# Kernel tuning notes

Hardware: AMD Instinct MI355X
Metric: run time of the kernel (lower is better)

The kernel has to match this reference:

```python
import jax, jax.numpy as jnp
import numpy as np

N_VERTS = 2562


def _uniform(key, shape, bound):
    return jax.random.uniform(key, shape, jnp.float32, -bound, bound)


def vert_align(feat, pos):
    # feat: [B,C,H,W]; pos: [B,N,3], xy in [-1,1] -> bilinear sample -> [B,N,C]
    B, C, H, W = feat.shape
    ft = jnp.transpose(feat, (0, 2, 3, 1))  # [B,H,W,C]
    x = (jnp.clip(pos[..., 0], -1.0, 1.0) + 1.0) * 0.5 * (W - 1)
    y = (jnp.clip(pos[..., 1], -1.0, 1.0) + 1.0) * 0.5 * (H - 1)
    x0 = jnp.floor(x)
    y0 = jnp.floor(y)
    x0i = x0.astype(jnp.int32)
    y0i = y0.astype(jnp.int32)
    x1i = jnp.minimum(x0i + 1, W - 1)
    y1i = jnp.minimum(y0i + 1, H - 1)
    wx = (x - x0)[..., None]
    wy = (y - y0)[..., None]
    b = jnp.arange(B)[:, None]
    f00 = ft[b, y0i, x0i]
    f01 = ft[b, y0i, x1i]
    f10 = ft[b, y1i, x0i]
    f11 = ft[b, y1i, x1i]
    return (f00 * (1 - wx) * (1 - wy) + f01 * wx * (1 - wy)
            + f10 * (1 - wx) * wy + f11 * wx * wy)


def graph_conv(x, adj, w0, w1):
    # relu(x @ w0 + adj @ (x @ w1))
    return jax.nn.relu(x @ w0 + jnp.einsum('bij,bjc->bic', adj, x @ w1))


def setup_inputs() -> dict:
    key = jax.random.key(0)
    ks = jax.random.split(key, 20)
    B, N = 8, N_VERTS
    inp = {
        'conv2_3': jax.random.normal(ks[0], (B, 256, 56, 56), jnp.float32),
        'conv3_4': jax.random.normal(ks[1], (B, 512, 28, 28), jnp.float32),
        'conv4_6': jax.random.normal(ks[2], (B, 1024, 14, 14), jnp.float32),
        'conv5_3': jax.random.normal(ks[3], (B, 2048, 7, 7), jnp.float32),
        # scaled so row sums are O(1), like a normalized dense adjacency
        'vertex_adjacency': jax.random.uniform(ks[4], (B, N, N), jnp.float32) * (2.0 / N),
        'vertex_positions': jax.random.uniform(ks[5], (B, N, 3), jnp.float32) * 2.0 - 1.0,
        'vertex_features': jax.random.normal(ks[6], (B, N, 128), jnp.float32),
    }
    # learned parameters (torch default / GraphConv uniform init)
    inp['w_lin0'] = _uniform(ks[7], (3840, 128), 1.0 / np.sqrt(3840))
    inp['b_lin0'] = _uniform(ks[8], (128,), 1.0 / np.sqrt(3840))
    inp['gc0_w0'] = _uniform(ks[9], (259, 131), 1.0 / np.sqrt(259))
    inp['gc0_w1'] = _uniform(ks[10], (259, 131), 1.0 / np.sqrt(259))
    inp['gc1_w0'] = _uniform(ks[11], (131, 128), 1.0 / np.sqrt(131))
    inp['gc1_w1'] = _uniform(ks[12], (131, 128), 1.0 / np.sqrt(131))
    inp['gc2_w0'] = _uniform(ks[13], (131, 128), 1.0 / np.sqrt(131))
    inp['gc2_w1'] = _uniform(ks[14], (131, 128), 1.0 / np.sqrt(131))
    inp['w_lin1'] = _uniform(ks[15], (128, 3), 1.0 / np.sqrt(128))
    inp['b_lin1'] = _uniform(ks[16], (3,), 1.0 / np.sqrt(128))
    return inp


def reference(conv2_3, conv3_4, conv4_6, conv5_3, vertex_adjacency,
              vertex_positions, vertex_features,
              w_lin0, b_lin0, gc0_w0, gc0_w1, gc1_w0, gc1_w1,
              gc2_w0, gc2_w1, w_lin1, b_lin1):
    verts = jnp.concatenate(
        [vert_align(f, vertex_positions)
         for f in (conv2_3, conv3_4, conv4_6, conv5_3)], axis=2)  # [B,N,3840]
    projected = verts @ w_lin0 + b_lin0                             # [B,N,128]
    vf = jnp.concatenate([vertex_features, vertex_positions, projected], axis=2)  # 259
    h = graph_conv(vf, vertex_adjacency, gc0_w0, gc0_w1)            # [B,N,131]
    h = jnp.concatenate([vertex_positions, h], axis=2)              # 134? no: 3+131=134 -- see note
    h = graph_conv(h[:, :, :131] if h.shape[2] != 131 else h, vertex_adjacency, gc1_w0, gc1_w1)
    h = jnp.concatenate([vertex_positions, h], axis=2)              # 131
    new_features = graph_conv(h, vertex_adjacency, gc2_w0, gc2_w1)  # [B,N,128]
    new_positions = vertex_positions + jnp.tanh(new_features @ w_lin1 + b_lin1)
    return new_positions, new_features
```

## Files before the change

kernel.cpp:

```cpp
#include <hip/hip_runtime.h>
#include <hip/hip_bf16.h>

typedef __attribute__((ext_vector_type(8))) short bf16x8;
typedef __attribute__((ext_vector_type(4))) float f32x4;
typedef long long i64;

static __device__ __forceinline__ float bflo(unsigned v){ return __uint_as_float(v << 16); }
static __device__ __forceinline__ float bfhi(unsigned v){ return __uint_as_float(v & 0xffff0000u); }
static __device__ __forceinline__ unsigned short f2bf(float f){
  unsigned u = __float_as_uint(f);
  u += 0x7FFFu + ((u >> 16) & 1u);
  return (unsigned short)(u >> 16);
}
static __device__ __forceinline__ unsigned f2e4m3(float x){
  unsigned b = __float_as_uint(x);
  unsigned s = (b >> 31) << 7;
  b &= 0x7fffffffu;
  if (b >= 0x43e80000u) return s | 0x7eu;
  if (b < 0x3c800000u)
    return s | (unsigned)rintf(__uint_as_float(b) * 512.f);
  unsigned b2 = b + 0x7ffffu + ((b >> 20) & 1u);
  return s | (((b2 >> 23) - 120u) << 3) | ((b2 >> 20) & 7u);
}
static __device__ __forceinline__ unsigned pk4_e4m3(float a, float b, float c, float d){
#if __has_builtin(__builtin_amdgcn_cvt_pk_fp8_f32)
  unsigned r = 0;
  r = (unsigned)__builtin_amdgcn_cvt_pk_fp8_f32(a, b, (int)r, false);
  r = (unsigned)__builtin_amdgcn_cvt_pk_fp8_f32(c, d, (int)r, true);
  return r;
#else
  return f2e4m3(a) | (f2e4m3(b) << 8) | (f2e4m3(c) << 16) | (f2e4m3(d) << 24);
#endif
}
static __device__ __forceinline__ void gload_lds16(const void* g, void* l){
  __builtin_amdgcn_global_load_lds((const __attribute__((address_space(1))) unsigned int*)g,
                                   (__attribute__((address_space(3))) unsigned int*)l, 16, 0, 0);
}

#define MFMA16(acc, a, b) (acc) = __builtin_amdgcn_mfma_f32_16x16x32_bf16((a),(b),(acc),0,0,0)
#define MFMA8(acc, a, b)  (acc) = __builtin_amdgcn_mfma_f32_16x16x32_fp8_fp8((a),(b),(acc),0,0,0)

#define NB    8
#define NVRT  2562
#define MP    2624
#define NRB2  82
#define NRB16 164
#define NKT8  21
#define KOCT  336
#define YO    ((size_t)KOCT*128*8)

#define G_B0 0ul
#define G_B1 3211264ul
#define G_B2 4014080ul
#define G_B3 4214784ul
#define G_TOT 4264960ul

struct PWArgs {
  const float* src[7];
  unsigned short* dst[7];
  int ksrc[7], nsrc[7];
};
__global__ void k_packw_all(PWArgs a)
{
  const int cb[8] = {0,491520,528384,565248,585728,606208,626688,647168};
  int g = blockIdx.x * 256 + threadIdx.x;
#pragma unroll
  for (int s = 0; s < 7; s++){
    if (g >= cb[s] && g < cb[s+1]){
      int li = g - cb[s];
      int k = li >> 7, c = li & 127;
      int ks = a.ksrc[s], ns = a.nsrc[s];
      float v = (k < ks) ? a.src[s][(size_t)k * ns + c] : 0.f;
      a.dst[s][((size_t)(k >> 3) * 128 + c) * 8 + (k & 7)] = f2bf(v);
    }
  }
}

__global__ __launch_bounds__(256) void k_gproj2(
    const float* __restrict__ c0m, const float* __restrict__ c1m,
    const float* __restrict__ c2m, const float* __restrict__ c3m,
    const unsigned short* __restrict__ wp,
    unsigned short* __restrict__ G)
{
  __shared__ f32x4 red[3][1024];
  int bx = blockIdx.x;
  int m, b, tile;
  if (bx < 784)      { m = 0; b = bx / 98;  tile = bx - b*98; }
  else if (bx < 984) { int l = bx-784;  m = 1; b = l / 25; tile = l - b*25; }
  else if (bx < 1040){ int l = bx-984;  m = 2; b = l / 7;  tile = l - b*7; }
  else               { int l = bx-1040; m = 3; b = l >> 1; tile = l & 1; }
  int C  = 256 << m;
  int HW = (m==0)?3136:(m==1)?784:(m==2)?196:49;
  const float* src = ((m==0)?c0m:(m==1)?c1m:(m==2)?c2m:c3m) + (size_t)b * C * HW;
  size_t gb = ((m==0)?G_B0:(m==1)?G_B1:(m==2)?G_B2:G_B3) + (size_t)b * HW * 128;
  int ko8 = (m==0)?0:(m==1)?32:(m==2)?96:224;

  int t = threadIdx.x, w = t >> 6, lane = t & 63;
  int l15 = lane & 15, l4 = lane >> 4;
  int hw0 = tile * 32;
  int ar0 = min(hw0 + l15, HW - 1);
  int ar1 = min(hw0 + 16 + l15, HW - 1);

  f32x4 acc[2][8];
#pragma unroll
  for (int i = 0; i < 2; i++)
#pragma unroll
    for (int j = 0; j < 8; j++) acc[i][j] = (f32x4){0,0,0,0};

  int kq = C >> 2;
  int kbeg = w * kq, klim = kbeg + kq;
  for (int kb = kbeg; kb < klim; kb += 32){
    bf16x8 a0, a1;
#pragma unroll
    for (int j = 0; j < 8; j++){
      int cc = kb + l4*8 + j;
      a0[j] = (short)f2bf(src[(size_t)cc * HW + ar0]);
      a1[j] = (short)f2bf(src[(size_t)cc * HW + ar1]);
    }
    size_t bo = ((size_t)(ko8 + (kb>>3) + l4) * 128 + l15) * 8;
#pragma unroll
    for (int cf = 0; cf < 8; cf++){
      bf16x8 bb = *(const bf16x8*)(wp + bo + cf*128);
      MFMA16(acc[0][cf], a0, bb);
      MFMA16(acc[1][cf], a1, bb);
    }
  }

  if (w){
#pragma unroll
    for (int rf = 0; rf < 2; rf++)
#pragma unroll
      for (int cf = 0; cf < 8; cf++)
        red[w-1][(rf*8+cf)*64 + lane] = acc[rf][cf];
  }
  __syncthreads();
  if (!w){
#pragma unroll
    for (int rf = 0; rf < 2; rf++)
#pragma unroll
      for (int cf = 0; cf < 8; cf++){
        int i = (rf*8+cf)*64 + lane;
        f32x4 s = acc[rf][cf] + red[0][i] + red[1][i] + red[2][i];
        int col = cf*16 + l15;
#pragma unroll
        for (int r = 0; r < 4; r++){
          int hw = hw0 + rf*16 + l4*4 + r;
          if (hw < HW) G[gb + (size_t)hw*128 + col] = f2bf(s[r]);
        }
      }
  }
}

__global__ void k_prep2(const float* __restrict__ vfeat, const float* __restrict__ pos,
                        const unsigned short* __restrict__ G,
                        const float* __restrict__ bias,
                        unsigned short* __restrict__ vf,
                        unsigned short* __restrict__ x1,
                        unsigned short* __restrict__ x2,
                        unsigned char* __restrict__ y1A,
                        unsigned char* __restrict__ y1B)
{
  int b = blockIdx.y;
  if (blockIdx.x == 0){
    unsigned long long* za = (unsigned long long*)(y1A + (size_t)b*YO + (size_t)328*128*8);
    unsigned long long* zb = (unsigned long long*)(y1B + (size_t)b*YO + (size_t)328*128*8);
    int i = threadIdx.x;
#pragma unroll
    for (int j = 0; j < 4; j++){ za[i*4+j] = 0; zb[i*4+j] = 0; }
  }
  int row = blockIdx.x * 4 + (threadIdx.x >> 6);
  int lane = threadIdx.x & 63;
  size_t vfo = ((size_t)b * MP + row) * 288;
  size_t xo  = ((size_t)b * MP + row) * 160;
  if (row < NVRT){
    size_t src = (size_t)b * NVRT + row;
    float px = fminf(fmaxf(pos[src*3 + 0], -1.f), 1.f);
    float py = fminf(fmaxf(pos[src*3 + 1], -1.f), 1.f);
    int c0 = lane * 2;
    float s0 = bias[c0], s1 = bias[c0 + 1];
#pragma unroll
    for (int m = 0; m < 4; m++){
      int W = 56 >> m;
      int HW = W * W;
      size_t gb = (m==0)?G_B0:(m==1)?G_B1:(m==2)?G_B2:G_B3;
      float gx = (px + 1.f) * 0.5f * (float)(W - 1);
      float gy = (py + 1.f) * 0.5f * (float)(W - 1);
      int x0 = (int)floorf(gx), y0 = (int)floorf(gy);
      float wx = gx - (float)x0, wy = gy - (float)y0;
      int x1i = min(x0 + 1, W - 1), y1i = min(y0 + 1, W - 1);
      const unsigned short* g = G + gb + (size_t)b * HW * 128;
      unsigned v00 = *(const unsigned*)(g + ((size_t)(y0 *W + x0 ))*128 + c0);
      unsigned v01 = *(const unsigned*)(g + ((size_t)(y0 *W + x1i))*128 + c0);
      unsigned v10 = *(const unsigned*)(g + ((size_t)(y1i*W + x0 ))*128 + c0);
      unsigned v11 = *(const unsigned*)(g + ((size_t)(y1i*W + x1i))*128 + c0);
      float w00 = (1.f-wx)*(1.f-wy), w01 = wx*(1.f-wy);
      float w10 = (1.f-wx)*wy,       w11 = wx*wy;
      s0 += w00*bflo(v00) + w01*bflo(v01) + w10*bflo(v10) + w11*bflo(v11);
      s1 += w00*bfhi(v00) + w01*bfhi(v01) + w10*bfhi(v10) + w11*bfhi(v11);
    }
    vf[vfo + 131 + c0]     = f2bf(s0);
    vf[vfo + 131 + c0 + 1] = f2bf(s1);
    float2 fv = *(const float2*)(vfeat + src*128 + c0);
    vf[vfo + c0]     = f2bf(fv.x);
    vf[vfo + c0 + 1] = f2bf(fv.y);
    if (lane < 3){
      unsigned short v = f2bf(pos[src*3 + lane]);
      vf[vfo + 128 + lane] = v;
      x1[xo + lane] = v;
      x2[xo + lane] = v;
    }
    if (lane >= 32 && lane < 61) vf[vfo + 259 + (lane - 32)] = 0;
    if (lane < 29){ x1[xo + 131 + lane] = 0; x2[xo + 131 + lane] = 0; }
  } else {
    for (int c = lane; c < 288; c += 64) vf[vfo + c] = 0;
    for (int c = lane; c < 160; c += 64){ x1[xo + c] = 0; x2[xo + c] = 0; }
  }
}

__global__ __launch_bounds__(256) void k_adjpack8(const float* __restrict__ adj,
                                                  unsigned char* __restrict__ adjP)
{
  int bid = blockIdx.x;
  int b = bid & 7, rb = bid >> 3;
  int t = threadIdx.x;
  int r = t >> 4, kseg = t & 15;
  int grow = rb*16 + r;
  bool rv = grow < NVRT;
  const float* arow = adj + ((size_t)b*NVRT + (rv ? grow : 0))*NVRT;
  unsigned char* tb = adjP + (((size_t)b*NRB16 + rb)*NKT8) * 2048;
  int tslot = 128*r + 8*(kseg ^ r);

#pragma unroll 3
  for (int kt = 0; kt < NKT8; ++kt){
    int gk = kt*128 + kseg*8;
    float v[8];
    if (rv && gk + 8 <= NVRT){
      float4 f0 = *(const float4*)(arow + gk);
      float4 f1 = *(const float4*)(arow + gk + 4);
      v[0]=f0.x; v[1]=f0.y; v[2]=f0.z; v[3]=f0.w;
      v[4]=f1.x; v[5]=f1.y; v[6]=f1.z; v[7]=f1.w;
    } else if (rv){
#pragma unroll
      for (int e = 0; e < 8; e++){ int k = gk + e; v[e] = (k < NVRT) ? arow[k] : 0.f; }
    } else {
#pragma unroll
      for (int e = 0; e < 8; e++) v[e] = 0.f;
    }
    unsigned lo = pk4_e4m3(v[0]*1024.f, v[1]*1024.f, v[2]*1024.f, v[3]*1024.f);
    unsigned hi = pk4_e4m3(v[4]*1024.f, v[5]*1024.f, v[6]*1024.f, v[7]*1024.f);
    unsigned long long q = (unsigned long long)lo | ((unsigned long long)hi << 32);
    *(unsigned long long*)(tb + (size_t)kt*2048 + tslot) = q;
  }
}

template<int KX>
__global__ __launch_bounds__(256) void k_y1(
    const unsigned short* __restrict__ x,
    const unsigned short* __restrict__ wp1,
    unsigned char* __restrict__ y1p8)
{
  int bid = blockIdx.x;
  int b = bid & 7, rb = (bid >> 3) * 32;
  int t = threadIdx.x, wave = t >> 6, lane = t & 63;
  int rf = wave & 1, ch = wave >> 1;
  int l15 = lane & 15, l4 = lane >> 4;
  f32x4 a1[4];
#pragma unroll
  for (int c = 0; c < 4; c++) a1[c] = (f32x4){0,0,0,0};
  int row = rb + rf*16 + l15;
  const unsigned short* xp = x + ((size_t)b * MP + row) * KX + l4 * 8;
#pragma unroll
  for (int kb = 0; kb < KX; kb += 32){
    bf16x8 a = *(const bf16x8*)(xp + kb);
    size_t bo = ((size_t)((kb>>3) + l4) * 128 + ch*64 + l15) * 8;
#pragma unroll
    for (int c = 0; c < 4; c++){
      bf16x8 b1 = *(const bf16x8*)(wp1 + bo + c*128);
      MFMA16(a1[c], a, b1);
    }
  }
  unsigned char* yb = y1p8 + (size_t)b * YO;
#pragma unroll
  for (int c = 0; c < 4; c++){
    int col = ch*64 + c*16 + l15;
    int orow0 = rb + rf*16 + l4*4;
    unsigned q = pk4_e4m3(a1[c][0], a1[c][1], a1[c][2], a1[c][3]);
    *(unsigned*)(yb + ((size_t)(orow0 >> 3) * 128 + col) * 8 + (orow0 & 7)) = q;
  }
}

template<int EPI, int KX>
__global__ __launch_bounds__(256) void k_adj8(
    const unsigned char* __restrict__ adjP,
    const unsigned char* __restrict__ y1in,
    const unsigned short* __restrict__ x,
    const unsigned short* __restrict__ wp0,
    const unsigned short* __restrict__ wp1n,
    unsigned char* __restrict__ y1out,
    const float* __restrict__ posg,
    unsigned short* __restrict__ xnext,
    float* __restrict__ outf,
    const float* __restrict__ wl1, const float* __restrict__ bl1,
    float* __restrict__ opos)
{
  __shared__ __align__(16) unsigned char abuf[2][2048];
  __shared__ unsigned short xbuf[EPI == 0 ? 16 : 1][168];
  __shared__ float hbuf[EPI == 1 ? 16 : 1][128];
  int bid = blockIdx.x;
  int b = bid & 7, rb = bid >> 3;
  int t = threadIdx.x, w = t >> 6, lane = t & 63;
  int l15 = lane & 15, l4 = lane >> 4;
  const unsigned char* tb = adjP + (((size_t)b*NRB16 + rb)*NKT8) * 2048;
  const unsigned char* yb = y1in + (size_t)b * YO;

  f32x4 acc[2], accW[2];
  acc[0] = (f32x4){0,0,0,0};  acc[1] = (f32x4){0,0,0,0};
  accW[0] = (f32x4){0,0,0,0}; accW[1] = (f32x4){0,0,0,0};

  auto stage = [&](int kt, int bufi){
    if (w < 2)
      gload_lds16(tb + (size_t)kt*2048 + w*1024 + lane*16, &abuf[bufi][w*1024]);
  };

  stage(0, 0);

  if (EPI == 0){
    if (t < 48){
      int r16 = t / 3, c = t - r16*3;
      int grow = rb*16 + r16;
      xbuf[r16][c] = (grow < NVRT) ? f2bf(posg[((size_t)b*NVRT + grow)*3 + c]) : 0;
    }
    {
      int r16 = t >> 4, c0 = 131 + (t & 15);
      xbuf[r16][c0] = 0;
      if (c0 + 16 < 168) xbuf[r16][c0 + 16] = 0;
      if (c0 + 32 < 168) xbuf[r16][c0 + 32] = 0;
    }
  }

  const unsigned short* xr = x + ((size_t)b*MP + rb*16 + l15)*KX + l4*8;
#pragma unroll
  for (int kb = 0; kb < KX; kb += 32){
    bf16x8 ax = *(const bf16x8*)(xr + kb);
    size_t bo = ((size_t)((kb>>3) + l4)*128 + w*32 + l15)*8;
    MFMA16(accW[0], ax, *(const bf16x8*)(wp0 + bo));
    MFMA16(accW[1], ax, *(const bf16x8*)(wp0 + bo + 128));
  }

  __syncthreads();

  for (int kt = 0; kt < NKT8; ++kt){
    int cur = kt & 1;
    if (kt < NKT8-1) stage(kt+1, cur ^ 1);
    const unsigned char* ab = &abuf[cur][0];
#pragma unroll
    for (int sel = 0; sel < 2; sel++){
#pragma unroll
      for (int ks = 0; ks < 2; ks++){
        int koct = sel*8 + ks*4 + l4;
        i64 a = *(const i64*)(ab + 128*l15 + 8*(koct ^ l15));
        const unsigned char* bp = yb + ((size_t)(kt*16 + koct)*128 + w*32 + l15)*8;
        i64 b0 = *(const i64*)(bp);
        i64 b1 = *(const i64*)(bp + 128);
        MFMA8(acc[0], a, b0);
        MFMA8(acc[1], a, b1);
      }
    }
    __syncthreads();
  }

#pragma unroll
  for (int cf = 0; cf < 2; cf++){
    int col = w*32 + cf*16 + l15;
#pragma unroll
    for (int r = 0; r < 4; r++){
      int row16 = l4*4 + r;
      int row = rb*16 + row16;
      float v = fmaxf(accW[cf][r] + acc[cf][r] * 0.0009765625f, 0.f);
      if (EPI == 0){
        unsigned short hb = f2bf(v);
        if (row < NVRT) xnext[((size_t)b*MP + row)*160 + 3 + col] = hb;
        xbuf[row16][3 + col] = hb;
      } else {
        if (row < NVRT) outf[((size_t)b*NVRT + row)*128 + col] = v;
        hbuf[row16][col] = v;
      }
    }
  }
  __syncthreads();

  if (EPI == 0){
    f32x4 accY[2];
    accY[0] = (f32x4){0,0,0,0}; accY[1] = (f32x4){0,0,0,0};
#pragma unroll
    for (int ks = 0; ks < 5; ks++){
      bf16x8 a = *(const bf16x8*)(&xbuf[l15][ks*32 + l4*8]);
      size_t bo = ((size_t)(ks*4 + l4)*128 + w*32 + l15)*8;
      MFMA16(accY[0], a, *(const bf16x8*)(wp1n + bo));
      MFMA16(accY[1], a, *(const bf16x8*)(wp1n + bo + 128));
    }
    unsigned char* yo = y1out + (size_t)b * YO;
#pragma unroll
    for (int cf = 0; cf < 2; cf++){
      int col = w*32 + cf*16 + l15;
      int orow0 = rb*16 + l4*4;
      unsigned q = pk4_e4m3(accY[cf][0], accY[cf][1], accY[cf][2], accY[cf][3]);
      *(unsigned*)(yo + ((size_t)(orow0 >> 3) * 128 + col) * 8 + (orow0 & 7)) = q;
    }
  } else {
#pragma unroll
    for (int rr = 0; rr < 4; rr++){
      int row16 = w*4 + rr;
      int grow = rb*16 + row16;
      if (grow < NVRT){
        int c0 = lane * 2;
        float v0 = hbuf[row16][c0], v1 = hbuf[row16][c0+1];
        float p[3];
#pragma unroll
        for (int j = 0; j < 3; j++){
          p[j] = v0 * wl1[c0*3 + j] + v1 * wl1[c0*3 + 3 + j];
#pragma unroll
          for (int off = 1; off < 64; off <<= 1)
            p[j] += __shfl_xor(p[j], off);
        }
        if (lane == 0){
          size_t po = ((size_t)b * NVRT + grow) * 3;
#pragma unroll
          for (int j = 0; j < 3; j++)
            opos[po + j] = posg[po + j] + tanhf(p[j] + bl1[j]);
        }
      }
    }
  }
}

extern "C" void kernel_launch(void* const* d_in, const int* in_sizes, int n_in,
                              void* d_out, int out_size, void* d_ws, size_t ws_size,
                              hipStream_t stream)
{
  const float* conv[4] = {(const float*)d_in[0], (const float*)d_in[1],
                          (const float*)d_in[2], (const float*)d_in[3]};
  const float* adj   = (const float*)d_in[4];
  const float* pos   = (const float*)d_in[5];
  const float* vfeat = (const float*)d_in[6];
  const float* wlin0 = (const float*)d_in[7];
  const float* blin0 = (const float*)d_in[8];
  const float* gw[6] = {(const float*)d_in[9],  (const float*)d_in[10],
                        (const float*)d_in[11], (const float*)d_in[12],
                        (const float*)d_in[13], (const float*)d_in[14]};
  const float* wlin1 = (const float*)d_in[15];
  const float* blin1 = (const float*)d_in[16];

  char* ws = (char*)d_ws;
  size_t off = 0;
  auto take = [&](size_t bytes)->char* {
    char* p = ws + off;
    off += (bytes + 255) & ~(size_t)255;
    return p;
  };
  unsigned short* G    = (unsigned short*)take(G_TOT * 2);
  unsigned char*  adjP = (unsigned char*)take((size_t)NB*NRB16*NKT8*2048);
  unsigned short* wl0p = (unsigned short*)take((size_t)3840*128*2);
  unsigned short* w0p0 = (unsigned short*)take((size_t)288*128*2);
  unsigned short* w1p0 = (unsigned short*)take((size_t)288*128*2);
  unsigned short* w0p1 = (unsigned short*)take((size_t)160*128*2);
  unsigned short* w1p1 = (unsigned short*)take((size_t)160*128*2);
  unsigned short* w0p2 = (unsigned short*)take((size_t)160*128*2);
  unsigned short* w1p2 = (unsigned short*)take((size_t)160*128*2);
  unsigned short* vf   = (unsigned short*)take((size_t)NB*MP*288*2);
  unsigned short* x1   = (unsigned short*)take((size_t)NB*MP*160*2);
  unsigned short* x2   = (unsigned short*)take((size_t)NB*MP*160*2);
  unsigned char*  y1A  = (unsigned char*)take((size_t)NB*YO);
  unsigned char*  y1B  = (unsigned char*)take((size_t)NB*YO);

  float* out_pos  = (float*)d_out;
  float* out_feat = out_pos + (size_t)NB*NVRT*3;

  PWArgs pw;
  pw.src[0]=wlin0; pw.dst[0]=wl0p; pw.ksrc[0]=3840; pw.nsrc[0]=128;
  pw.src[1]=gw[0]; pw.dst[1]=w0p0; pw.ksrc[1]=259;  pw.nsrc[1]=131;
  pw.src[2]=gw[1]; pw.dst[2]=w1p0; pw.ksrc[2]=259;  pw.nsrc[2]=131;
  pw.src[3]=gw[2]; pw.dst[3]=w0p1; pw.ksrc[3]=131;  pw.nsrc[3]=128;
  pw.src[4]=gw[3]; pw.dst[4]=w1p1; pw.ksrc[4]=131;  pw.nsrc[4]=128;
  pw.src[5]=gw[4]; pw.dst[5]=w0p2; pw.ksrc[5]=131;  pw.nsrc[5]=128;
  pw.src[6]=gw[5]; pw.dst[6]=w1p2; pw.ksrc[6]=131;  pw.nsrc[6]=128;
  k_packw_all<<<2528, 256, 0, stream>>>(pw);
  k_gproj2<<<1056, 256, 0, stream>>>(conv[0], conv[1], conv[2], conv[3], wl0p, G);
  k_prep2<<<dim3(MP/4, NB), 256, 0, stream>>>(vfeat, pos, G, blin0, vf, x1, x2, y1A, y1B);
  k_y1<288><<<NRB2*NB, 256, 0, stream>>>(vf, w1p0, y1A);
  k_adjpack8<<<NRB16*NB, 256, 0, stream>>>(adj, adjP);
  k_adj8<0,288><<<NRB16*NB, 256, 0, stream>>>(adjP, y1A, vf, w0p0, w1p1, y1B, pos,
                                              x1, nullptr, nullptr, nullptr, nullptr);
  k_adj8<0,160><<<NRB16*NB, 256, 0, stream>>>(adjP, y1B, x1, w0p1, w1p2, y1A, pos,
                                              x2, nullptr, nullptr, nullptr, nullptr);
  k_adj8<1,160><<<NRB16*NB, 256, 0, stream>>>(adjP, y1A, x2, w0p2, nullptr, nullptr, pos,
                                              nullptr, out_feat, wlin1, blin1, out_pos);
  (void)in_sizes; (void)n_in; (void)out_size; (void)ws_size;
}
```

Before: 263.1 us.

## Split adjacency fp8 packing across gproj, prep and y1 launches

```diff
diff --git a/kernel.cpp b/kernel.cpp
--- a/kernel.cpp
+++ b/kernel.cpp
@@ -49,11 +49,49 @@
 #define KOCT  336
 #define YO    ((size_t)KOCT*128*8)
 
+#define AP_G 512
+#define AP_P 512
+#define AP_Y 288
+
 #define G_B0 0ul
 #define G_B1 3211264ul
 #define G_B2 4014080ul
 #define G_B3 4214784ul
 #define G_TOT 4264960ul
+
+static __device__ __forceinline__ void adjpack_slab(int slab, const float* __restrict__ adj,
+                                                    unsigned char* __restrict__ adjP, int t)
+{
+  int b = slab & 7, rb = slab >> 3;
+  int r = t >> 4, kseg = t & 15;
+  int grow = rb*16 + r;
+  bool rv = grow < NVRT;
+  const float* arow = adj + ((size_t)b*NVRT + (rv ? grow : 0))*NVRT;
+  unsigned char* tb = adjP + (((size_t)b*NRB16 + rb)*NKT8) * 2048;
+  int tslot = 128*r + 8*(kseg ^ r);
+
+#pragma unroll 3
+  for (int kt = 0; kt < NKT8; ++kt){
+    int gk = kt*128 + kseg*8;
+    float v[8];
+    if (rv && gk + 8 <= NVRT){
+      float4 f0 = *(const float4*)(arow + gk);
+      float4 f1 = *(const float4*)(arow + gk + 4);
+      v[0]=f0.x; v[1]=f0.y; v[2]=f0.z; v[3]=f0.w;
+      v[4]=f1.x; v[5]=f1.y; v[6]=f1.z; v[7]=f1.w;
+    } else if (rv){
+#pragma unroll
+      for (int e = 0; e < 8; e++){ int k = gk + e; v[e] = (k < NVRT) ? arow[k] : 0.f; }
+    } else {
+#pragma unroll
+      for (int e = 0; e < 8; e++) v[e] = 0.f;
+    }
+    unsigned lo = pk4_e4m3(v[0]*1024.f, v[1]*1024.f, v[2]*1024.f, v[3]*1024.f);
+    unsigned hi = pk4_e4m3(v[4]*1024.f, v[5]*1024.f, v[6]*1024.f, v[7]*1024.f);
+    unsigned long long q = (unsigned long long)lo | ((unsigned long long)hi << 32);
+    *(unsigned long long*)(tb + (size_t)kt*2048 + tslot) = q;
+  }
+}
 
 struct PWArgs {
   const float* src[7];
@@ -76,14 +114,17 @@
   }
 }
 
-__global__ __launch_bounds__(256) void k_gproj2(
+__global__ __launch_bounds__(256) void k_par_gproj(
+    const float* __restrict__ adjSrc, unsigned char* __restrict__ adjP,
     const float* __restrict__ c0m, const float* __restrict__ c1m,
     const float* __restrict__ c2m, const float* __restrict__ c3m,
     const unsigned short* __restrict__ wp,
     unsigned short* __restrict__ G)
 {
   __shared__ f32x4 red[3][1024];
-  int bx = blockIdx.x;
+  int bid = blockIdx.x;
+  if (bid < AP_G){ adjpack_slab(bid, adjSrc, adjP, threadIdx.x); return; }
+  int bx = bid - AP_G;
   int m, b, tile;
   if (bx < 784)      { m = 0; b = bx / 98;  tile = bx - b*98; }
   else if (bx < 984) { int l = bx-784;  m = 1; b = l / 25; tile = l - b*25; }
@@ -151,24 +192,29 @@
   }
 }
 
-__global__ void k_prep2(const float* __restrict__ vfeat, const float* __restrict__ pos,
-                        const unsigned short* __restrict__ G,
-                        const float* __restrict__ bias,
-                        unsigned short* __restrict__ vf,
-                        unsigned short* __restrict__ x1,
-                        unsigned short* __restrict__ x2,
-                        unsigned char* __restrict__ y1A,
-                        unsigned char* __restrict__ y1B)
-{
-  int b = blockIdx.y;
-  if (blockIdx.x == 0){
+__global__ __launch_bounds__(256) void k_par_prep(
+    const float* __restrict__ adjSrc, unsigned char* __restrict__ adjP,
+    const float* __restrict__ vfeat, const float* __restrict__ pos,
+    const unsigned short* __restrict__ G,
+    const float* __restrict__ bias,
+    unsigned short* __restrict__ vf,
+    unsigned short* __restrict__ x1,
+    unsigned short* __restrict__ x2,
+    unsigned char* __restrict__ y1A,
+    unsigned char* __restrict__ y1B)
+{
+  int bid = blockIdx.x;
+  if (bid < AP_P){ adjpack_slab(AP_G + bid, adjSrc, adjP, threadIdx.x); return; }
+  int idx = bid - AP_P;
+  int b = idx & 7, rblk = idx >> 3;
+  if (rblk == 0){
     unsigned long long* za = (unsigned long long*)(y1A + (size_t)b*YO + (size_t)328*128*8);
     unsigned long long* zb = (unsigned long long*)(y1B + (size_t)b*YO + (size_t)328*128*8);
     int i = threadIdx.x;
 #pragma unroll
     for (int j = 0; j < 4; j++){ za[i*4+j] = 0; zb[i*4+j] = 0; }
   }
-  int row = blockIdx.x * 4 + (threadIdx.x >> 6);
+  int row = rblk * 4 + (threadIdx.x >> 6);
   int lane = threadIdx.x & 63;
   size_t vfo = ((size_t)b * MP + row) * 288;
   size_t xo  = ((size_t)b * MP + row) * 160;
@@ -217,50 +263,16 @@
   }
 }
 
-__global__ __launch_bounds__(256) void k_adjpack8(const float* __restrict__ adj,
-                                                  unsigned char* __restrict__ adjP)
-{
-  int bid = blockIdx.x;
-  int b = bid & 7, rb = bid >> 3;
-  int t = threadIdx.x;
-  int r = t >> 4, kseg = t & 15;
-  int grow = rb*16 + r;
-  bool rv = grow < NVRT;
-  const float* arow = adj + ((size_t)b*NVRT + (rv ? grow : 0))*NVRT;
-  unsigned char* tb = adjP + (((size_t)b*NRB16 + rb)*NKT8) * 2048;
-  int tslot = 128*r + 8*(kseg ^ r);
-
-#pragma unroll 3
-  for (int kt = 0; kt < NKT8; ++kt){
-    int gk = kt*128 + kseg*8;
-    float v[8];
-    if (rv && gk + 8 <= NVRT){
-      float4 f0 = *(const float4*)(arow + gk);
-      float4 f1 = *(const float4*)(arow + gk + 4);
-      v[0]=f0.x; v[1]=f0.y; v[2]=f0.z; v[3]=f0.w;
-      v[4]=f1.x; v[5]=f1.y; v[6]=f1.z; v[7]=f1.w;
-    } else if (rv){
-#pragma unroll
-      for (int e = 0; e < 8; e++){ int k = gk + e; v[e] = (k < NVRT) ? arow[k] : 0.f; }
-    } else {
-#pragma unroll
-      for (int e = 0; e < 8; e++) v[e] = 0.f;
-    }
-    unsigned lo = pk4_e4m3(v[0]*1024.f, v[1]*1024.f, v[2]*1024.f, v[3]*1024.f);
-    unsigned hi = pk4_e4m3(v[4]*1024.f, v[5]*1024.f, v[6]*1024.f, v[7]*1024.f);
-    unsigned long long q = (unsigned long long)lo | ((unsigned long long)hi << 32);
-    *(unsigned long long*)(tb + (size_t)kt*2048 + tslot) = q;
-  }
-}
-
-template<int KX>
-__global__ __launch_bounds__(256) void k_y1(
+__global__ __launch_bounds__(256) void k_par_y1(
+    const float* __restrict__ adjSrc, unsigned char* __restrict__ adjP,
     const unsigned short* __restrict__ x,
     const unsigned short* __restrict__ wp1,
     unsigned char* __restrict__ y1p8)
 {
   int bid = blockIdx.x;
-  int b = bid & 7, rb = (bid >> 3) * 32;
+  if (bid < AP_Y){ adjpack_slab(AP_G + AP_P + bid, adjSrc, adjP, threadIdx.x); return; }
+  int yid = bid - AP_Y;
+  int b = yid & 7, rb = (yid >> 3) * 32;
   int t = threadIdx.x, wave = t >> 6, lane = t & 63;
   int rf = wave & 1, ch = wave >> 1;
   int l15 = lane & 15, l4 = lane >> 4;
@@ -268,9 +280,9 @@
 #pragma unroll
   for (int c = 0; c < 4; c++) a1[c] = (f32x4){0,0,0,0};
   int row = rb + rf*16 + l15;
-  const unsigned short* xp = x + ((size_t)b * MP + row) * KX + l4 * 8;
-#pragma unroll
-  for (int kb = 0; kb < KX; kb += 32){
+  const unsigned short* xp = x + ((size_t)b * MP + row) * 288 + l4 * 8;
+#pragma unroll
+  for (int kb = 0; kb < 288; kb += 32){
     bf16x8 a = *(const bf16x8*)(xp + kb);
     size_t bo = ((size_t)((kb>>3) + l4) * 128 + ch*64 + l15) * 8;
 #pragma unroll
@@ -485,10 +497,11 @@
   pw.src[5]=gw[4]; pw.dst[5]=w0p2; pw.ksrc[5]=131;  pw.nsrc[5]=128;
   pw.src[6]=gw[5]; pw.dst[6]=w1p2; pw.ksrc[6]=131;  pw.nsrc[6]=128;
   k_packw_all<<<2528, 256, 0, stream>>>(pw);
-  k_gproj2<<<1056, 256, 0, stream>>>(conv[0], conv[1], conv[2], conv[3], wl0p, G);
-  k_prep2<<<dim3(MP/4, NB), 256, 0, stream>>>(vfeat, pos, G, blin0, vf, x1, x2, y1A, y1B);
-  k_y1<288><<<NRB2*NB, 256, 0, stream>>>(vf, w1p0, y1A);
-  k_adjpack8<<<NRB16*NB, 256, 0, stream>>>(adj, adjP);
+  k_par_gproj<<<AP_G + 1056, 256, 0, stream>>>(adj, adjP,
+                                               conv[0], conv[1], conv[2], conv[3], wl0p, G);
+  k_par_prep<<<AP_P + 656*NB, 256, 0, stream>>>(adj, adjP,
+                                                vfeat, pos, G, blin0, vf, x1, x2, y1A, y1B);
+  k_par_y1<<<AP_Y + NRB2*NB, 256, 0, stream>>>(adj, adjP, vf, w1p0, y1A);
   k_adj8<0,288><<<NRB16*NB, 256, 0, stream>>>(adjP, y1A, vf, w0p0, w1p1, y1B, pos,
                                               x1, nullptr, nullptr, nullptr, nullptr);
   k_adj8<0,160><<<NRB16*NB, 256, 0, stream>>>(adjP, y1B, x1, w0p1, w1p2, y1A, pos,
```

Measured after the change: 259.7 us. No clear change (-1.3%).

## Fuse y1, adjacency packing and three graph-conv stages into one persistent kernel

Applied to the files above, without the earlier changes.

```diff
diff --git a/kernel.cpp b/kernel.cpp
--- a/kernel.cpp
+++ b/kernel.cpp
@@ -48,12 +48,281 @@
 #define NKT8  21
 #define KOCT  336
 #define YO    ((size_t)KOCT*128*8)
+#define MEGA_GRID 656
 
 #define G_B0 0ul
 #define G_B1 3211264ul
 #define G_B2 4014080ul
 #define G_B3 4214784ul
 #define G_TOT 4264960ul
+
+static __device__ __forceinline__ void gsync(unsigned* ctr){
+  __syncthreads();
+  if (threadIdx.x == 0){
+    __threadfence();
+    atomicAdd(ctr, 1u);
+    while (__hip_atomic_load(ctr, __ATOMIC_ACQUIRE, __HIP_MEMORY_SCOPE_AGENT) < (unsigned)gridDim.x)
+      __builtin_amdgcn_s_sleep(2);
+  }
+  __syncthreads();
+}
+
+static __device__ __forceinline__ void adjpack_slab(int slab, const float* __restrict__ adj,
+                                                    unsigned char* __restrict__ adjP, int t)
+{
+  int b = slab & 7, rb = slab >> 3;
+  int r = t >> 4, kseg = t & 15;
+  int grow = rb*16 + r;
+  bool rv = grow < NVRT;
+  const float* arow = adj + ((size_t)b*NVRT + (rv ? grow : 0))*NVRT;
+  unsigned char* tb = adjP + (((size_t)b*NRB16 + rb)*NKT8) * 2048;
+  int tslot = 128*r + 8*(kseg ^ r);
+
+#pragma unroll 3
+  for (int kt = 0; kt < NKT8; ++kt){
+    int gk = kt*128 + kseg*8;
+    float v[8];
+    if (rv && gk + 8 <= NVRT){
+      float4 f0 = *(const float4*)(arow + gk);
+      float4 f1 = *(const float4*)(arow + gk + 4);
+      v[0]=f0.x; v[1]=f0.y; v[2]=f0.z; v[3]=f0.w;
+      v[4]=f1.x; v[5]=f1.y; v[6]=f1.z; v[7]=f1.w;
+    } else if (rv){
+#pragma unroll
+      for (int e = 0; e < 8; e++){ int k = gk + e; v[e] = (k < NVRT) ? arow[k] : 0.f; }
+    } else {
+#pragma unroll
+      for (int e = 0; e < 8; e++) v[e] = 0.f;
+    }
+    unsigned lo = pk4_e4m3(v[0]*1024.f, v[1]*1024.f, v[2]*1024.f, v[3]*1024.f);
+    unsigned hi = pk4_e4m3(v[4]*1024.f, v[5]*1024.f, v[6]*1024.f, v[7]*1024.f);
+    unsigned long long q = (unsigned long long)lo | ((unsigned long long)hi << 32);
+    *(unsigned long long*)(tb + (size_t)kt*2048 + tslot) = q;
+  }
+}
+
+static __device__ __forceinline__ void y1_body(int yid,
+    const unsigned short* __restrict__ x,
+    const unsigned short* __restrict__ wp1,
+    unsigned char* __restrict__ y1p8)
+{
+  int b = yid & 7, rb = (yid >> 3) * 32;
+  int t = threadIdx.x, wave = t >> 6, lane = t & 63;
+  int rf = wave & 1, ch = wave >> 1;
+  int l15 = lane & 15, l4 = lane >> 4;
+  f32x4 a1[4];
+#pragma unroll
+  for (int c = 0; c < 4; c++) a1[c] = (f32x4){0,0,0,0};
+  int row = rb + rf*16 + l15;
+  const unsigned short* xp = x + ((size_t)b * MP + row) * 288 + l4 * 8;
+#pragma unroll
+  for (int kb = 0; kb < 288; kb += 32){
+    bf16x8 a = *(const bf16x8*)(xp + kb);
+    size_t bo = ((size_t)((kb>>3) + l4) * 128 + ch*64 + l15) * 8;
+#pragma unroll
+    for (int c = 0; c < 4; c++){
+      bf16x8 b1 = *(const bf16x8*)(wp1 + bo + c*128);
+      MFMA16(a1[c], a, b1);
+    }
+  }
+  unsigned char* yb = y1p8 + (size_t)b * YO;
+#pragma unroll
+  for (int c = 0; c < 4; c++){
+    int col = ch*64 + c*16 + l15;
+    int orow0 = rb + rf*16 + l4*4;
+    unsigned q = pk4_e4m3(a1[c][0], a1[c][1], a1[c][2], a1[c][3]);
+    *(unsigned*)(yb + ((size_t)(orow0 >> 3) * 128 + col) * 8 + (orow0 & 7)) = q;
+  }
+}
+
+template<int EPI, int KX>
+static __device__ __forceinline__ void adj8_body(int slab,
+    unsigned char (&abuf)[2][2048],
+    unsigned short (&xbuf)[16][168],
+    float (&hbuf)[16][128],
+    const unsigned char* __restrict__ adjP,
+    const unsigned char* __restrict__ y1in,
+    const unsigned short* __restrict__ x,
+    const unsigned short* __restrict__ wp0,
+    const unsigned short* __restrict__ wp1n,
+    unsigned char* __restrict__ y1out,
+    const float* __restrict__ posg,
+    unsigned short* __restrict__ xnext,
+    float* __restrict__ outf,
+    const float* __restrict__ wl1, const float* __restrict__ bl1,
+    float* __restrict__ opos)
+{
+  int b = slab & 7, rb = slab >> 3;
+  int t = threadIdx.x, w = t >> 6, lane = t & 63;
+  int l15 = lane & 15, l4 = lane >> 4;
+  const unsigned char* tb = adjP + (((size_t)b*NRB16 + rb)*NKT8) * 2048;
+  const unsigned char* yb = y1in + (size_t)b * YO;
+
+  f32x4 acc[2], accW[2];
+  acc[0] = (f32x4){0,0,0,0};  acc[1] = (f32x4){0,0,0,0};
+  accW[0] = (f32x4){0,0,0,0}; accW[1] = (f32x4){0,0,0,0};
+
+  auto stage = [&](int kt, int bufi){
+    if (w < 2)
+      gload_lds16(tb + (size_t)kt*2048 + w*1024 + lane*16, &abuf[bufi][w*1024]);
+  };
+
+  stage(0, 0);
+
+  if (EPI == 0){
+    if (t < 48){
+      int r16 = t / 3, c = t - r16*3;
+      int grow = rb*16 + r16;
+      xbuf[r16][c] = (grow < NVRT) ? f2bf(posg[((size_t)b*NVRT + grow)*3 + c]) : 0;
+    }
+    {
+      int r16 = t >> 4, c0 = 131 + (t & 15);
+      xbuf[r16][c0] = 0;
+      if (c0 + 16 < 168) xbuf[r16][c0 + 16] = 0;
+      if (c0 + 32 < 168) xbuf[r16][c0 + 32] = 0;
+    }
+  }
+
+  const unsigned short* xr = x + ((size_t)b*MP + rb*16 + l15)*KX + l4*8;
+#pragma unroll
+  for (int kb = 0; kb < KX; kb += 32){
+    bf16x8 ax = *(const bf16x8*)(xr + kb);
+    size_t bo = ((size_t)((kb>>3) + l4)*128 + w*32 + l15)*8;
+    MFMA16(accW[0], ax, *(const bf16x8*)(wp0 + bo));
+    MFMA16(accW[1], ax, *(const bf16x8*)(wp0 + bo + 128));
+  }
+
+  __syncthreads();
+
+  for (int kt = 0; kt < NKT8; ++kt){
+    int cur = kt & 1;
+    if (kt < NKT8-1) stage(kt+1, cur ^ 1);
+    const unsigned char* ab = &abuf[cur][0];
+#pragma unroll
+    for (int sel = 0; sel < 2; sel++){
+#pragma unroll
+      for (int ks = 0; ks < 2; ks++){
+        int koct = sel*8 + ks*4 + l4;
+        i64 a = *(const i64*)(ab + 128*l15 + 8*(koct ^ l15));
+        const unsigned char* bp = yb + ((size_t)(kt*16 + koct)*128 + w*32 + l15)*8;
+        i64 b0 = *(const i64*)(bp);
+        i64 b1 = *(const i64*)(bp + 128);
+        MFMA8(acc[0], a, b0);
+        MFMA8(acc[1], a, b1);
+      }
+    }
+    __syncthreads();
+  }
+
+#pragma unroll
+  for (int cf = 0; cf < 2; cf++){
+    int col = w*32 + cf*16 + l15;
+#pragma unroll
+    for (int r = 0; r < 4; r++){
+      int row16 = l4*4 + r;
+      int row = rb*16 + row16;
+      float v = fmaxf(accW[cf][r] + acc[cf][r] * 0.0009765625f, 0.f);
+      if (EPI == 0){
+        unsigned short hb = f2bf(v);
+        if (row < NVRT) xnext[((size_t)b*MP + row)*160 + 3 + col] = hb;
+        xbuf[row16][3 + col] = hb;
+      } else {
+        if (row < NVRT) outf[((size_t)b*NVRT + row)*128 + col] = v;
+        hbuf[row16][col] = v;
+      }
+    }
+  }
+  __syncthreads();
+
+  if (EPI == 0){
+    f32x4 accY[2];
+    accY[0] = (f32x4){0,0,0,0}; accY[1] = (f32x4){0,0,0,0};
+#pragma unroll
+    for (int ks = 0; ks < 5; ks++){
+      bf16x8 a = *(const bf16x8*)(&xbuf[l15][ks*32 + l4*8]);
+      size_t bo = ((size_t)(ks*4 + l4)*128 + w*32 + l15)*8;
+      MFMA16(accY[0], a, *(const bf16x8*)(wp1n + bo));
+      MFMA16(accY[1], a, *(const bf16x8*)(wp1n + bo + 128));
+    }
+    unsigned char* yo = y1out + (size_t)b * YO;
+#pragma unroll
+    for (int cf = 0; cf < 2; cf++){
+      int col = w*32 + cf*16 + l15;
+      int orow0 = rb*16 + l4*4;
+      unsigned q = pk4_e4m3(accY[cf][0], accY[cf][1], accY[cf][2], accY[cf][3]);
+      *(unsigned*)(yo + ((size_t)(orow0 >> 3) * 128 + col) * 8 + (orow0 & 7)) = q;
+    }
+  } else {
+#pragma unroll
+    for (int rr = 0; rr < 4; rr++){
+      int row16 = w*4 + rr;
+      int grow = rb*16 + row16;
+      if (grow < NVRT){
+        int c0 = lane * 2;
+        float v0 = hbuf[row16][c0], v1 = hbuf[row16][c0+1];
+        float p[3];
+#pragma unroll
+        for (int j = 0; j < 3; j++){
+          p[j] = v0 * wl1[c0*3 + j] + v1 * wl1[c0*3 + 3 + j];
+#pragma unroll
+          for (int off = 1; off < 64; off <<= 1)
+            p[j] += __shfl_xor(p[j], off);
+        }
+        if (lane == 0){
+          size_t po = ((size_t)b * NVRT + grow) * 3;
+#pragma unroll
+          for (int j = 0; j < 3; j++)
+            opos[po + j] = posg[po + j] + tanhf(p[j] + bl1[j]);
+        }
+      }
+    }
+  }
+}
+
+__global__ __launch_bounds__(256, 3) void k_mega(
+    const float* __restrict__ adjSrc, unsigned char* __restrict__ adjP,
+    const unsigned short* __restrict__ vf,
+    const unsigned short* __restrict__ w1p0, const unsigned short* __restrict__ w0p0,
+    const unsigned short* __restrict__ w1p1, const unsigned short* __restrict__ w0p1,
+    const unsigned short* __restrict__ w1p2, const unsigned short* __restrict__ w0p2,
+    unsigned char* __restrict__ y1A, unsigned char* __restrict__ y1B,
+    unsigned short* __restrict__ x1, unsigned short* __restrict__ x2,
+    const float* __restrict__ pos, float* __restrict__ out_feat,
+    const float* __restrict__ wl1, const float* __restrict__ bl1,
+    float* __restrict__ out_pos,
+    unsigned* __restrict__ ctrs)
+{
+  __shared__ __align__(16) unsigned char abuf[2][2048];
+  __shared__ unsigned short xbuf[16][168];
+  __shared__ float hbuf[16][128];
+  int bid = blockIdx.x;
+  int s0 = 2*bid, s1 = 2*bid + 1;
+
+  y1_body(bid, vf, w1p0, y1A);
+  adjpack_slab(s0, adjSrc, adjP, threadIdx.x);
+  adjpack_slab(s1, adjSrc, adjP, threadIdx.x);
+  gsync(&ctrs[0]);
+
+  adj8_body<0,288>(s0, abuf, xbuf, hbuf, adjP, y1A, vf, w0p0, w1p1, y1B, pos, x1,
+                   nullptr, nullptr, nullptr, nullptr);
+  __syncthreads();
+  adj8_body<0,288>(s1, abuf, xbuf, hbuf, adjP, y1A, vf, w0p0, w1p1, y1B, pos, x1,
+                   nullptr, nullptr, nullptr, nullptr);
+  gsync(&ctrs[1]);
+
+  adj8_body<0,160>(s0, abuf, xbuf, hbuf, adjP, y1B, x1, w0p1, w1p2, y1A, pos, x2,
+                   nullptr, nullptr, nullptr, nullptr);
+  __syncthreads();
+  adj8_body<0,160>(s1, abuf, xbuf, hbuf, adjP, y1B, x1, w0p1, w1p2, y1A, pos, x2,
+                   nullptr, nullptr, nullptr, nullptr);
+  gsync(&ctrs[2]);
+
+  adj8_body<1,160>(s0, abuf, xbuf, hbuf, adjP, y1A, x2, w0p2, nullptr, nullptr, pos,
+                   nullptr, out_feat, wl1, bl1, out_pos);
+  __syncthreads();
+  adj8_body<1,160>(s1, abuf, xbuf, hbuf, adjP, y1A, x2, w0p2, nullptr, nullptr, pos,
+                   nullptr, out_feat, wl1, bl1, out_pos);
+}
 
 struct PWArgs {
   const float* src[7];
@@ -158,7 +427,8 @@
                         unsigned short* __restrict__ x1,
                         unsigned short* __restrict__ x2,
                         unsigned char* __restrict__ y1A,
-                        unsigned char* __restrict__ y1B)
+                        unsigned char* __restrict__ y1B,
+                        unsigned* __restrict__ ctrs)
 {
   int b = blockIdx.y;
   if (blockIdx.x == 0){
@@ -167,6 +437,7 @@
     int i = threadIdx.x;
 #pragma unroll
     for (int j = 0; j < 4; j++){ za[i*4+j] = 0; zb[i*4+j] = 0; }
+    if (b == 0 && threadIdx.x < 8) ctrs[threadIdx.x] = 0;
   }
   int row = blockIdx.x * 4 + (threadIdx.x >> 6);
   int lane = threadIdx.x & 63;
@@ -214,223 +485,6 @@
   } else {
     for (int c = lane; c < 288; c += 64) vf[vfo + c] = 0;
     for (int c = lane; c < 160; c += 64){ x1[xo + c] = 0; x2[xo + c] = 0; }
-  }
-}
-
-__global__ __launch_bounds__(256) void k_adjpack8(const float* __restrict__ adj,
-                                                  unsigned char* __restrict__ adjP)
-{
-  int bid = blockIdx.x;
-  int b = bid & 7, rb = bid >> 3;
-  int t = threadIdx.x;
-  int r = t >> 4, kseg = t & 15;
-  int grow = rb*16 + r;
-  bool rv = grow < NVRT;
-  const float* arow = adj + ((size_t)b*NVRT + (rv ? grow : 0))*NVRT;
-  unsigned char* tb = adjP + (((size_t)b*NRB16 + rb)*NKT8) * 2048;
-  int tslot = 128*r + 8*(kseg ^ r);
-
-#pragma unroll 3
-  for (int kt = 0; kt < NKT8; ++kt){
-    int gk = kt*128 + kseg*8;
-    float v[8];
-    if (rv && gk + 8 <= NVRT){
-      float4 f0 = *(const float4*)(arow + gk);
-      float4 f1 = *(const float4*)(arow + gk + 4);
-      v[0]=f0.x; v[1]=f0.y; v[2]=f0.z; v[3]=f0.w;
-      v[4]=f1.x; v[5]=f1.y; v[6]=f1.z; v[7]=f1.w;
-    } else if (rv){
-#pragma unroll
-      for (int e = 0; e < 8; e++){ int k = gk + e; v[e] = (k < NVRT) ? arow[k] : 0.f; }
-    } else {
-#pragma unroll
-      for (int e = 0; e < 8; e++) v[e] = 0.f;
-    }
-    unsigned lo = pk4_e4m3(v[0]*1024.f, v[1]*1024.f, v[2]*1024.f, v[3]*1024.f);
-    unsigned hi = pk4_e4m3(v[4]*1024.f, v[5]*1024.f, v[6]*1024.f, v[7]*1024.f);
-    unsigned long long q = (unsigned long long)lo | ((unsigned long long)hi << 32);
-    *(unsigned long long*)(tb + (size_t)kt*2048 + tslot) = q;
-  }
-}
-
-template<int KX>
-__global__ __launch_bounds__(256) void k_y1(
-    const unsigned short* __restrict__ x,
-    const unsigned short* __restrict__ wp1,
-    unsigned char* __restrict__ y1p8)
-{
-  int bid = blockIdx.x;
-  int b = bid & 7, rb = (bid >> 3) * 32;
-  int t = threadIdx.x, wave = t >> 6, lane = t & 63;
-  int rf = wave & 1, ch = wave >> 1;
-  int l15 = lane & 15, l4 = lane >> 4;
-  f32x4 a1[4];
-#pragma unroll
-  for (int c = 0; c < 4; c++) a1[c] = (f32x4){0,0,0,0};
-  int row = rb + rf*16 + l15;
-  const unsigned short* xp = x + ((size_t)b * MP + row) * KX + l4 * 8;
-#pragma unroll
-  for (int kb = 0; kb < KX; kb += 32){
-    bf16x8 a = *(const bf16x8*)(xp + kb);
-    size_t bo = ((size_t)((kb>>3) + l4) * 128 + ch*64 + l15) * 8;
-#pragma unroll
-    for (int c = 0; c < 4; c++){
-      bf16x8 b1 = *(const bf16x8*)(wp1 + bo + c*128);
-      MFMA16(a1[c], a, b1);
-    }
-  }
-  unsigned char* yb = y1p8 + (size_t)b * YO;
-#pragma unroll
-  for (int c = 0; c < 4; c++){
-    int col = ch*64 + c*16 + l15;
-    int orow0 = rb + rf*16 + l4*4;
-    unsigned q = pk4_e4m3(a1[c][0], a1[c][1], a1[c][2], a1[c][3]);
-    *(unsigned*)(yb + ((size_t)(orow0 >> 3) * 128 + col) * 8 + (orow0 & 7)) = q;
-  }
-}
-
-template<int EPI, int KX>
-__global__ __launch_bounds__(256) void k_adj8(
-    const unsigned char* __restrict__ adjP,
-    const unsigned char* __restrict__ y1in,
-    const unsigned short* __restrict__ x,
-    const unsigned short* __restrict__ wp0,
-    const unsigned short* __restrict__ wp1n,
-    unsigned char* __restrict__ y1out,
-    const float* __restrict__ posg,
-    unsigned short* __restrict__ xnext,
-    float* __restrict__ outf,
-    const float* __restrict__ wl1, const float* __restrict__ bl1,
-    float* __restrict__ opos)
-{
-  __shared__ __align__(16) unsigned char abuf[2][2048];
-  __shared__ unsigned short xbuf[EPI == 0 ? 16 : 1][168];
-  __shared__ float hbuf[EPI == 1 ? 16 : 1][128];
-  int bid = blockIdx.x;
-  int b = bid & 7, rb = bid >> 3;
-  int t = threadIdx.x, w = t >> 6, lane = t & 63;
-  int l15 = lane & 15, l4 = lane >> 4;
-  const unsigned char* tb = adjP + (((size_t)b*NRB16 + rb)*NKT8) * 2048;
-  const unsigned char* yb = y1in + (size_t)b * YO;
-
-  f32x4 acc[2], accW[2];
-  acc[0] = (f32x4){0,0,0,0};  acc[1] = (f32x4){0,0,0,0};
-  accW[0] = (f32x4){0,0,0,0}; accW[1] = (f32x4){0,0,0,0};
-
-  auto stage = [&](int kt, int bufi){
-    if (w < 2)
-      gload_lds16(tb + (size_t)kt*2048 + w*1024 + lane*16, &abuf[bufi][w*1024]);
-  };
-
-  stage(0, 0);
-
-  if (EPI == 0){
-    if (t < 48){
-      int r16 = t / 3, c = t - r16*3;
-      int grow = rb*16 + r16;
-      xbuf[r16][c] = (grow < NVRT) ? f2bf(posg[((size_t)b*NVRT + grow)*3 + c]) : 0;
-    }
-    {
-      int r16 = t >> 4, c0 = 131 + (t & 15);
-      xbuf[r16][c0] = 0;
-      if (c0 + 16 < 168) xbuf[r16][c0 + 16] = 0;
-      if (c0 + 32 < 168) xbuf[r16][c0 + 32] = 0;
-    }
-  }
-
-  const unsigned short* xr = x + ((size_t)b*MP + rb*16 + l15)*KX + l4*8;
-#pragma unroll
-  for (int kb = 0; kb < KX; kb += 32){
-    bf16x8 ax = *(const bf16x8*)(xr + kb);
-    size_t bo = ((size_t)((kb>>3) + l4)*128 + w*32 + l15)*8;
-    MFMA16(accW[0], ax, *(const bf16x8*)(wp0 + bo));
-    MFMA16(accW[1], ax, *(const bf16x8*)(wp0 + bo + 128));
-  }
-
-  __syncthreads();
-
-  for (int kt = 0; kt < NKT8; ++kt){
-    int cur = kt & 1;
-    if (kt < NKT8-1) stage(kt+1, cur ^ 1);
-    const unsigned char* ab = &abuf[cur][0];
-#pragma unroll
-    for (int sel = 0; sel < 2; sel++){
-#pragma unroll
-      for (int ks = 0; ks < 2; ks++){
-        int koct = sel*8 + ks*4 + l4;
-        i64 a = *(const i64*)(ab + 128*l15 + 8*(koct ^ l15));
-        const unsigned char* bp = yb + ((size_t)(kt*16 + koct)*128 + w*32 + l15)*8;
-        i64 b0 = *(const i64*)(bp);
-        i64 b1 = *(const i64*)(bp + 128);
-        MFMA8(acc[0], a, b0);
-        MFMA8(acc[1], a, b1);
-      }
-    }
-    __syncthreads();
-  }
-
-#pragma unroll
-  for (int cf = 0; cf < 2; cf++){
-    int col = w*32 + cf*16 + l15;
-#pragma unroll
-    for (int r = 0; r < 4; r++){
-      int row16 = l4*4 + r;
-      int row = rb*16 + row16;
-      float v = fmaxf(accW[cf][r] + acc[cf][r] * 0.0009765625f, 0.f);
-      if (EPI == 0){
-        unsigned short hb = f2bf(v);
-        if (row < NVRT) xnext[((size_t)b*MP + row)*160 + 3 + col] = hb;
-        xbuf[row16][3 + col] = hb;
-      } else {
-        if (row < NVRT) outf[((size_t)b*NVRT + row)*128 + col] = v;
-        hbuf[row16][col] = v;
-      }
-    }
-  }
-  __syncthreads();
-
-  if (EPI == 0){
-    f32x4 accY[2];
-    accY[0] = (f32x4){0,0,0,0}; accY[1] = (f32x4){0,0,0,0};
-#pragma unroll
-    for (int ks = 0; ks < 5; ks++){
-      bf16x8 a = *(const bf16x8*)(&xbuf[l15][ks*32 + l4*8]);
-      size_t bo = ((size_t)(ks*4 + l4)*128 + w*32 + l15)*8;
-      MFMA16(accY[0], a, *(const bf16x8*)(wp1n + bo));
-      MFMA16(accY[1], a, *(const bf16x8*)(wp1n + bo + 128));
-    }
-    unsigned char* yo = y1out + (size_t)b * YO;
-#pragma unroll
-    for (int cf = 0; cf < 2; cf++){
-      int col = w*32 + cf*16 + l15;
-      int orow0 = rb*16 + l4*4;
-      unsigned q = pk4_e4m3(accY[cf][0], accY[cf][1], accY[cf][2], accY[cf][3]);
-      *(unsigned*)(yo + ((size_t)(orow0 >> 3) * 128 + col) * 8 + (orow0 & 7)) = q;
-    }
-  } else {
-#pragma unroll
-    for (int rr = 0; rr < 4; rr++){
-      int row16 = w*4 + rr;
-      int grow = rb*16 + row16;
-      if (grow < NVRT){
-        int c0 = lane * 2;
-        float v0 = hbuf[row16][c0], v1 = hbuf[row16][c0+1];
-        float p[3];
-#pragma unroll
-        for (int j = 0; j < 3; j++){
-          p[j] = v0 * wl1[c0*3 + j] + v1 * wl1[c0*3 + 3 + j];
-#pragma unroll
-          for (int off = 1; off < 64; off <<= 1)
-            p[j] += __shfl_xor(p[j], off);
-        }
-        if (lane == 0){
-          size_t po = ((size_t)b * NVRT + grow) * 3;
-#pragma unroll
-          for (int j = 0; j < 3; j++)
-            opos[po + j] = posg[po + j] + tanhf(p[j] + bl1[j]);
-        }
-      }
-    }
   }
 }
 
@@ -472,6 +526,7 @@
   unsigned short* x2   = (unsigned short*)take((size_t)NB*MP*160*2);
   unsigned char*  y1A  = (unsigned char*)take((size_t)NB*YO);
   unsigned char*  y1B  = (unsigned char*)take((size_t)NB*YO);
+  unsigned*       ctrs = (unsigned*)take(256);
 
   float* out_pos  = (float*)d_out;
   float* out_feat = out_pos + (size_t)NB*NVRT*3;
@@ -486,14 +541,10 @@
   pw.src[6]=gw[5]; pw.dst[6]=w1p2; pw.ksrc[6]=131;  pw.nsrc[6]=128;
   k_packw_all<<<2528, 256, 0, stream>>>(pw);
   k_gproj2<<<1056, 256, 0, stream>>>(conv[0], conv[1], conv[2], conv[3], wl0p, G);
-  k_prep2<<<dim3(MP/4, NB), 256, 0, stream>>>(vfeat, pos, G, blin0, vf, x1, x2, y1A, y1B);
-  k_y1<288><<<NRB2*NB, 256, 0, stream>>>(vf, w1p0, y1A);
-  k_adjpack8<<<NRB16*NB, 256, 0, stream>>>(adj, adjP);
-  k_adj8<0,288><<<NRB16*NB, 256, 0, stream>>>(adjP, y1A, vf, w0p0, w1p1, y1B, pos,
-                                              x1, nullptr, nullptr, nullptr, nullptr);
-  k_adj8<0,160><<<NRB16*NB, 256, 0, stream>>>(adjP, y1B, x1, w0p1, w1p2, y1A, pos,
-                                              x2, nullptr, nullptr, nullptr, nullptr);
-  k_adj8<1,160><<<NRB16*NB, 256, 0, stream>>>(adjP, y1A, x2, w0p2, nullptr, nullptr, pos,
-                                              nullptr, out_feat, wlin1, blin1, out_pos);
+  k_prep2<<<dim3(MP/4, NB), 256, 0, stream>>>(vfeat, pos, G, blin0, vf, x1, x2, y1A, y1B, ctrs);
+  k_mega<<<MEGA_GRID, 256, 0, stream>>>(adj, adjP, vf,
+                                        w1p0, w0p0, w1p1, w0p1, w1p2, w0p2,
+                                        y1A, y1B, x1, x2,
+                                        pos, out_feat, wlin1, blin1, out_pos, ctrs);
   (void)in_sizes; (void)n_in; (void)out_size; (void)ws_size;
 }
```

Result: slower. 1.038 ms (+294.5%).
